# Kernel tuning notes

Hardware: AMD Instinct MI355X
Metric: run time of the kernel (lower is better)

Reference implementation:

```python
import jax, jax.numpy as jnp
import numpy as np

C = 10  # cluster_num
EMB = 64

def setup_inputs() -> dict:
    key = jax.random.key(0)
    ks = jax.random.split(key, 12)
    B, N, D = 8, 4096, 1024
    n_classes = 1
    data = jax.random.normal(ks[0], (B, N, D), dtype=jnp.float32)
    labels = jax.random.randint(ks[1], (B, N), 0, C, dtype=jnp.int32)
    s = 0.02
    return {
        "data": data,
        "labels": labels,
        # embedding_net: Conv2d(1024,64,1) == linear on feature dim
        "W1": jax.random.normal(ks[2], (EMB, D), dtype=jnp.float32) * s,
        "b1": jnp.zeros((EMB,), dtype=jnp.float32),
        # attention MLP: Linear(64,32) -> tanh -> Linear(32,1)
        "Wa1": jax.random.normal(ks[3], (32, EMB), dtype=jnp.float32) * s,
        "ba1": jnp.zeros((32,), dtype=jnp.float32),
        "Wa2": jax.random.normal(ks[4], (1, 32), dtype=jnp.float32) * s,
        "ba2": jnp.zeros((1,), dtype=jnp.float32),
        # fc6: Linear(64,32) -> ReLU -> (Dropout eval=identity) -> Linear(32,n_classes)
        "Wf1": jax.random.normal(ks[5], (32, EMB), dtype=jnp.float32) * s,
        "bf1": jnp.zeros((32,), dtype=jnp.float32),
        "Wf2": jax.random.normal(ks[6], (n_classes, 32), dtype=jnp.float32) * s,
        "bf2": jnp.zeros((n_classes,), dtype=jnp.float32),
    }

def _masked_softmax(x, mask):
    # faithful to the module's numeric trick
    x_masked = x * mask + (1.0 - 1.0 / (mask + 1e-5))
    x_max = jnp.max(x_masked, axis=1, keepdims=True)
    x_exp = jnp.exp(x - x_max) * mask
    return x_exp / jnp.sum(x_exp, axis=1, keepdims=True)

def reference(data, labels, W1, b1, Wa1, ba1, Wa2, ba2, Wf1, bf1, Wf2, bf2):
    B, N, D = data.shape
    # per-patch 1x1-conv embed + ReLU: [B,N,64]
    e = jax.nn.relu(jnp.einsum('bnd,ed->bne', data, W1) + b1)
    # ragged per-cluster mean (AdaptiveAvgPool over each cluster's patches)
    seg = (labels.astype(jnp.int32) + jnp.arange(B, dtype=jnp.int32)[:, None] * C).reshape(-1)
    sums = jax.ops.segment_sum(e.reshape(B * N, EMB), seg, num_segments=B * C)
    counts = jax.ops.segment_sum(jnp.ones((B * N,), dtype=jnp.float32), seg, num_segments=B * C)
    sums = sums.reshape(B, C, EMB)
    counts = counts.reshape(B, C)
    mask = (counts > 0).astype(jnp.float32)
    h = sums / jnp.maximum(counts, 1.0)[..., None]  # [B,C,64]
    # attention scores over clusters
    a = jnp.einsum('bce,oe->bco', jnp.tanh(jnp.einsum('bce,he->bch', h, Wa1) + ba1), Wa2) + ba2
    A = _masked_softmax(a[..., 0], mask)  # [B,C]
    M = jnp.einsum('bc,bce->be', A, h)    # [B,64]
    # fc6 (dropout is identity at inference)
    logits = jax.nn.relu(M @ Wf1.T + bf1) @ Wf2.T + bf2
    return logits
```

## Files before the change

kernel.cpp:

```cpp
#include <hip/hip_runtime.h>

#define NC 10
#define EMB 64
#define DD 1024
#define NP 4096
#define NB 8

__global__ __launch_bounds__(256) void embed_seg_kernel(
    const float* __restrict__ data, const int* __restrict__ labels,
    const float* __restrict__ W1, const float* __restrict__ b1,
    float* __restrict__ sums, float* __restrict__ counts)
{
    __shared__ float As[64][66];
    __shared__ float Ws[64][66];
    __shared__ float csum[NC][EMB];
    __shared__ float ccnt[NC];
    __shared__ int   labs[64];

    const int t  = threadIdx.x;
    const int b  = blockIdx.x >> 6;
    const int p0 = (blockIdx.x & 63) << 6;

    for (int i = t; i < NC * EMB; i += 256) (&csum[0][0])[i] = 0.f;
    if (t < NC) ccnt[t] = 0.f;
    if (t < 64) labs[t] = labels[b * NP + p0 + t];

    const float* Ab = data + ((size_t)(b * NP + p0)) * DD;

    const int tx = t & 15;
    const int ty = t >> 4;
    const int lr = t >> 4;
    const int lc = (t & 15) << 2;

    float bias[4];
#pragma unroll
    for (int j = 0; j < 4; ++j) bias[j] = b1[(tx << 2) + j];

    float acc[4][4] = {};

    for (int kk = 0; kk < DD; kk += 64) {
        __syncthreads();
#pragma unroll
        for (int i = 0; i < 4; ++i) {
            const int r = lr + (i << 4);
            *(float4*)&As[r][lc] = *(const float4*)(Ab + (size_t)r * DD + kk + lc);
            *(float4*)&Ws[r][lc] = *(const float4*)(W1 + (size_t)r * DD + kk + lc);
        }
        __syncthreads();
#pragma unroll
        for (int k2 = 0; k2 < 32; ++k2) {
            const int k = k2 << 1;
            float2 av[4], wv[4];
#pragma unroll
            for (int i = 0; i < 4; ++i) {
                av[i] = *(const float2*)&As[(ty << 2) + i][k];
                wv[i] = *(const float2*)&Ws[(tx << 2) + i][k];
            }
#pragma unroll
            for (int i = 0; i < 4; ++i)
#pragma unroll
                for (int j = 0; j < 4; ++j) {
                    acc[i][j] = fmaf(av[i].x, wv[j].x, acc[i][j]);
                    acc[i][j] = fmaf(av[i].y, wv[j].y, acc[i][j]);
                }
        }
    }

    __syncthreads();
#pragma unroll
    for (int i = 0; i < 4; ++i) {
        const int lab = labs[(ty << 2) + i];
#pragma unroll
        for (int j = 0; j < 4; ++j) {
            float v = acc[i][j] + bias[j];
            v = v > 0.f ? v : 0.f;
            atomicAdd(&csum[lab][(tx << 2) + j], v);
        }
    }
    if (t < 64) atomicAdd(&ccnt[labs[t]], 1.0f);
    __syncthreads();
    for (int i = t; i < NC * EMB; i += 256)
        atomicAdd(&sums[b * NC * EMB + i], (&csum[0][0])[i]);
    if (t < NC) atomicAdd(&counts[b * NC + t], ccnt[t]);
}

__global__ __launch_bounds__(128) void head_kernel(
    const float* __restrict__ sums, const float* __restrict__ counts,
    const float* __restrict__ Wa1, const float* __restrict__ ba1,
    const float* __restrict__ Wa2, const float* __restrict__ ba2,
    const float* __restrict__ Wf1, const float* __restrict__ bf1,
    const float* __restrict__ Wf2, const float* __restrict__ bf2,
    float* __restrict__ out)
{
    __shared__ float h[NC][EMB];
    __shared__ float mask[NC];
    __shared__ float att[NC][32];
    __shared__ float a_s[NC];
    __shared__ float A_s[NC];
    __shared__ float M_s[EMB];
    __shared__ float f_s[32];

    const int b = blockIdx.x;
    const int t = threadIdx.x;

    if (t < NC) {
        float cnt = counts[b * NC + t];
        mask[t] = cnt > 0.f ? 1.f : 0.f;
    }
    for (int i = t; i < NC * EMB; i += 128) {
        int c = i >> 6;
        float cnt = counts[b * NC + c];
        (&h[0][0])[i] = sums[b * NC * EMB + i] / fmaxf(cnt, 1.f);
    }
    __syncthreads();

    for (int task = t; task < NC * 32; task += 128) {
        int c = task >> 5, hh = task & 31;
        float s = ba1[hh];
        for (int e = 0; e < EMB; ++e) s = fmaf(Wa1[hh * EMB + e], h[c][e], s);
        att[c][hh] = tanhf(s);
    }
    __syncthreads();

    if (t < NC) {
        float s = ba2[0];
        for (int hh = 0; hh < 32; ++hh) s = fmaf(Wa2[hh], att[t][hh], s);
        a_s[t] = s;
    }
    __syncthreads();

    if (t == 0) {
        float xmax = -1e30f;
        for (int c = 0; c < NC; ++c) {
            float xm = a_s[c] * mask[c] + (1.0f - 1.0f / (mask[c] + 1e-5f));
            xmax = fmaxf(xmax, xm);
        }
        float ex[NC], ssum = 0.f;
        for (int c = 0; c < NC; ++c) {
            ex[c] = expf(a_s[c] - xmax) * mask[c];
            ssum += ex[c];
        }
        for (int c = 0; c < NC; ++c) A_s[c] = ex[c] / ssum;
    }
    __syncthreads();

    if (t < EMB) {
        float s = 0.f;
        for (int c = 0; c < NC; ++c) s = fmaf(A_s[c], h[c][t], s);
        M_s[t] = s;
    }
    __syncthreads();

    if (t < 32) {
        float s = bf1[t];
        for (int e = 0; e < EMB; ++e) s = fmaf(Wf1[t * EMB + e], M_s[e], s);
        f_s[t] = fmaxf(s, 0.f);
    }
    __syncthreads();

    if (t == 0) {
        float s = bf2[0];
        for (int hh = 0; hh < 32; ++hh) s = fmaf(Wf2[hh], f_s[hh], s);
        out[b] = s;
    }
}

extern "C" void kernel_launch(void* const* d_in, const int* in_sizes, int n_in,
                              void* d_out, int out_size, void* d_ws, size_t ws_size,
                              hipStream_t stream)
{
    const float* data   = (const float*)d_in[0];
    const int*   labels = (const int*)  d_in[1];
    const float* W1     = (const float*)d_in[2];
    const float* b1     = (const float*)d_in[3];
    const float* Wa1    = (const float*)d_in[4];
    const float* ba1    = (const float*)d_in[5];
    const float* Wa2    = (const float*)d_in[6];
    const float* ba2    = (const float*)d_in[7];
    const float* Wf1    = (const float*)d_in[8];
    const float* bf1    = (const float*)d_in[9];
    const float* Wf2    = (const float*)d_in[10];
    const float* bf2    = (const float*)d_in[11];

    float* sums   = (float*)d_ws;
    float* counts = sums + NB * NC * EMB;

    hipMemsetAsync(d_ws, 0, (size_t)(NB * NC * EMB + NB * NC) * sizeof(float), stream);

    embed_seg_kernel<<<NB * 64, 256, 0, stream>>>(data, labels, W1, b1, sums, counts);
    head_kernel<<<NB, 128, 0, stream>>>(sums, counts, Wa1, ba1, Wa2, ba2,
                                        Wf1, bf1, Wf2, bf2, (float*)d_out);
}
```

Measured before the change: 315.4 us.

## Broadcast W1 via wave-uniform scalar loads and give each lane one row

Restructures the embedding GEMM so each wave owns 8 output channels and each lane one patch row. W1 is read directly from global memory with wave-uniform addresses (readfirstlane), so it can use scalar loads instead of being staged in LDS. The block grows to 512 threads and only the data tile goes through shared memory. This removes W1 LDS staging and reads but relies on scalar cache throughput for the weights and carries more atomics per block.

Measured after the change: 304.7 us. -3.4%, faster.

```diff
diff --git a/kernel.cpp b/kernel.cpp
--- a/kernel.cpp
+++ b/kernel.cpp
@@ -6,80 +6,67 @@
 #define NP 4096
 #define NB 8
 
-__global__ __launch_bounds__(256) void embed_seg_kernel(
+__global__ __launch_bounds__(512, 2) void embed_seg_kernel(
     const float* __restrict__ data, const int* __restrict__ labels,
     const float* __restrict__ W1, const float* __restrict__ b1,
     float* __restrict__ sums, float* __restrict__ counts)
 {
-    __shared__ float As[64][66];
-    __shared__ float Ws[64][66];
+    __shared__ float As[64][68];
     __shared__ float csum[NC][EMB];
     __shared__ float ccnt[NC];
     __shared__ int   labs[64];
 
-    const int t  = threadIdx.x;
-    const int b  = blockIdx.x >> 6;
-    const int p0 = (blockIdx.x & 63) << 6;
+    const int t    = threadIdx.x;
+    const int lane = t & 63;
+    const int w    = t >> 6;
+    const int b    = blockIdx.x >> 6;
+    const int p0   = (blockIdx.x & 63) << 6;
 
-    for (int i = t; i < NC * EMB; i += 256) (&csum[0][0])[i] = 0.f;
+    for (int i = t; i < NC * EMB; i += 512) (&csum[0][0])[i] = 0.f;
     if (t < NC) ccnt[t] = 0.f;
     if (t < 64) labs[t] = labels[b * NP + p0 + t];
 
-    const float* Ab = data + ((size_t)(b * NP + p0)) * DD;
+    const int we = __builtin_amdgcn_readfirstlane(w << 3);
+    const float* __restrict__ Wb = W1 + (size_t)we * DD;
 
-    const int tx = t & 15;
-    const int ty = t >> 4;
-    const int lr = t >> 4;
-    const int lc = (t & 15) << 2;
+    const float* Ab = data + (size_t)(b * NP + p0) * DD;
 
-    float bias[4];
-#pragma unroll
-    for (int j = 0; j < 4; ++j) bias[j] = b1[(tx << 2) + j];
+    const int srow = t >> 3;
+    const int scol = (t & 7) << 3;
 
-    float acc[4][4] = {};
+    float acc[8] = {};
 
     for (int kk = 0; kk < DD; kk += 64) {
         __syncthreads();
+        float4 v0 = *(const float4*)(Ab + (size_t)srow * DD + kk + scol);
+        float4 v1 = *(const float4*)(Ab + (size_t)srow * DD + kk + scol + 4);
+        *(float4*)&As[srow][scol]     = v0;
+        *(float4*)&As[srow][scol + 4] = v1;
+        __syncthreads();
+#pragma unroll 2
+        for (int kq = 0; kq < 16; ++kq) {
+            const float4 av = *(const float4*)&As[lane][kq << 2];
 #pragma unroll
-        for (int i = 0; i < 4; ++i) {
-            const int r = lr + (i << 4);
-            *(float4*)&As[r][lc] = *(const float4*)(Ab + (size_t)r * DD + kk + lc);
-            *(float4*)&Ws[r][lc] = *(const float4*)(W1 + (size_t)r * DD + kk + lc);
-        }
-        __syncthreads();
-#pragma unroll
-        for (int k2 = 0; k2 < 32; ++k2) {
-            const int k = k2 << 1;
-            float2 av[4], wv[4];
-#pragma unroll
-            for (int i = 0; i < 4; ++i) {
-                av[i] = *(const float2*)&As[(ty << 2) + i][k];
-                wv[i] = *(const float2*)&Ws[(tx << 2) + i][k];
+            for (int e = 0; e < 8; ++e) {
+                const float4 wv = *(const float4*)(Wb + (size_t)e * DD + kk + (kq << 2));
+                acc[e] = fmaf(av.x, wv.x, acc[e]);
+                acc[e] = fmaf(av.y, wv.y, acc[e]);
+                acc[e] = fmaf(av.z, wv.z, acc[e]);
+                acc[e] = fmaf(av.w, wv.w, acc[e]);
             }
-#pragma unroll
-            for (int i = 0; i < 4; ++i)
-#pragma unroll
-                for (int j = 0; j < 4; ++j) {
-                    acc[i][j] = fmaf(av[i].x, wv[j].x, acc[i][j]);
-                    acc[i][j] = fmaf(av[i].y, wv[j].y, acc[i][j]);
-                }
         }
     }
 
     __syncthreads();
+    const int lab = labs[lane];
 #pragma unroll
-    for (int i = 0; i < 4; ++i) {
-        const int lab = labs[(ty << 2) + i];
-#pragma unroll
-        for (int j = 0; j < 4; ++j) {
-            float v = acc[i][j] + bias[j];
-            v = v > 0.f ? v : 0.f;
-            atomicAdd(&csum[lab][(tx << 2) + j], v);
-        }
+    for (int e = 0; e < 8; ++e) {
+        float vv = fmaxf(acc[e] + b1[we + e], 0.f);
+        atomicAdd(&csum[lab][we + e], vv);
     }
-    if (t < 64) atomicAdd(&ccnt[labs[t]], 1.0f);
+    if (w == 0) atomicAdd(&ccnt[lab], 1.0f);
     __syncthreads();
-    for (int i = t; i < NC * EMB; i += 256)
+    for (int i = t; i < NC * EMB; i += 512)
         atomicAdd(&sums[b * NC * EMB + i], (&csum[0][0])[i]);
     if (t < NC) atomicAdd(&counts[b * NC + t], ccnt[t]);
 }
@@ -187,7 +174,7 @@
 
     hipMemsetAsync(d_ws, 0, (size_t)(NB * NC * EMB + NB * NC) * sizeof(float), stream);
 
-    embed_seg_kernel<<<NB * 64, 256, 0, stream>>>(data, labels, W1, b1, sums, counts);
+    embed_seg_kernel<<<NB * 64, 512, 0, stream>>>(data, labels, W1, b1, sums, counts);
     head_kernel<<<NB, 128, 0, stream>>>(sums, counts, Wa1, ba1, Wa2, ba2,
                                         Wf1, bf1, Wf2, bf2, (float*)d_out);
 }
```
